# Kernel tuning notes

Hardware: AMD Instinct MI355X
Metric: run time of the kernel (lower is better)

Reference implementation:

```python
import jax, jax.numpy as jnp
import numpy as np

VOCAB = 50257
N_EMBD = 640
BLOCK = 256
B = 16


def setup_inputs() -> dict:
    key = jax.random.key(0)
    ks = jax.random.split(key, 8)
    std = 0.02
    return {
        "idx": jax.random.randint(ks[0], (B, BLOCK), 0, VOCAB, dtype=jnp.int64 if jax.config.jax_enable_x64 else jnp.int32),
        "w_embed": jax.random.normal(ks[1], (VOCAB, N_EMBD), jnp.float32) * std,
        "w_pos": jax.random.normal(ks[2], (BLOCK, N_EMBD), jnp.float32) * std,
        "wq": jax.random.normal(ks[3], (N_EMBD, N_EMBD), jnp.float32) * std,
        "wk": jax.random.normal(ks[4], (N_EMBD, N_EMBD), jnp.float32) * std,
        "wv": jax.random.normal(ks[5], (N_EMBD, N_EMBD), jnp.float32) * std,
        "w_out": jax.random.normal(ks[6], (VOCAB, N_EMBD), jnp.float32) * std,
        "b_out": jnp.zeros((VOCAB,), jnp.float32),
    }


def reference(idx, w_embed, w_pos, wq, wk, wv, w_out, b_out):
    # idx: (B, T) token ids. Dropout is identity (eval mode).
    Bt, T = idx.shape
    x = w_embed[idx] + w_pos[:T]                      # (B, T, D)
    q = jnp.einsum('btd,ed->bte', x, wq)              # torch Linear: x @ W.T
    k = jnp.einsum('btd,ed->bte', x, wk)
    v = jnp.einsum('btd,ed->bte', x, wv)
    scale = jnp.asarray(N_EMBD ** 0.5, x.dtype)
    scores = jnp.einsum('btd,bsd->bts', q, k) / scale  # (B, T, T)
    causal = jnp.triu(jnp.ones((T, T), bool), k=1)     # True above diagonal
    scores = jnp.where(causal, jnp.asarray(-jnp.inf, scores.dtype), scores)
    attn = jax.nn.softmax(scores, axis=-1)
    attn_out = jnp.einsum('bts,bsd->btd', attn, v)     # (B, T, D)
    logits = jnp.einsum('btd,vd->btv', attn_out, w_out) + b_out  # (B, T, V)
    return logits
```

## Files before the change

### kernel.cpp

```cpp
#include <hip/hip_runtime.h>
#include <hip/hip_bf16.h>
#include <stdint.h>

#define VOCAB 50257
#define VPAD  50432
#define DIM   640
#define SEQ   256
#define NBATCH 16
#define MROWS 4096

using bf16 = __hip_bfloat16;
typedef __attribute__((ext_vector_type(8))) short short8;
typedef __attribute__((ext_vector_type(4))) float f32x4;
struct bf16x4 { bf16 a, b, c, d; };

__device__ __forceinline__ void gld_lds16(const void* g, void* l) {
  __builtin_amdgcn_global_load_lds(
      (const __attribute__((address_space(1))) void*)g,
      (__attribute__((address_space(3))) void*)l, 16, 0, 0);
}

#define BAR() asm volatile("s_barrier" ::: "memory")
#define VMC0() asm volatile("s_waitcnt vmcnt(0)" ::: "memory")

__global__ void embed_kernel(const int* __restrict__ idx,
                             const float* __restrict__ we,
                             const float* __restrict__ wp,
                             bf16* __restrict__ xb) {
  int row = blockIdx.x;
  int t = row & (SEQ - 1);
  int tok = idx[row];
  const float* src = we + (long)tok * DIM;
  const float* pos = wp + (long)t * DIM;
  for (int d = threadIdx.x * 4; d < DIM; d += blockDim.x * 4) {
    float4 s = *(const float4*)(src + d);
    float4 p = *(const float4*)(pos + d);
    bf16x4 o = { __float2bfloat16(s.x + p.x), __float2bfloat16(s.y + p.y),
                 __float2bfloat16(s.z + p.z), __float2bfloat16(s.w + p.w) };
    *(bf16x4*)(xb + (long)row * DIM + d) = o;
  }
}

__global__ void conv4_kernel(const float* __restrict__ src, bf16* __restrict__ dst,
                             long n_src, long n_dst) {
  long i = ((long)blockIdx.x * blockDim.x + threadIdx.x) * 4;
  long stride = (long)gridDim.x * blockDim.x * 4;
  for (; i < n_dst; i += stride) {
    float4 v = (i < n_src) ? *(const float4*)(src + i) : make_float4(0.f, 0.f, 0.f, 0.f);
    bf16x4 o = { __float2bfloat16(v.x), __float2bfloat16(v.y),
                 __float2bfloat16(v.z), __float2bfloat16(v.w) };
    *(bf16x4*)(dst + i) = o;
  }
}

__global__ void transpose_v(const bf16* __restrict__ v, bf16* __restrict__ vt) {
  long i = (long)blockIdx.x * blockDim.x + threadIdx.x;
  if (i >= (long)NBATCH * DIM * SEQ) return;
  int t = (int)(i & (SEQ - 1));
  long be = i >> 8;
  int e = (int)(be % DIM);
  int b = (int)(be / DIM);
  vt[i] = v[((long)b * SEQ + t) * DIM + e];
}

__global__ void softmax_kernel(const float* __restrict__ sc, bf16* __restrict__ p) {
  int wid = threadIdx.x >> 6, lane = threadIdx.x & 63;
  int row = blockIdx.x * 4 + wid;
  int t = row & (SEQ - 1);
  const float* srow = sc + (long)row * SEQ;
  const float rsc = 0.03952847075210474f;
  float v[4];
  float mx = -1e30f;
#pragma unroll
  for (int i = 0; i < 4; ++i) {
    int s = lane + 64 * i;
    v[i] = (s <= t) ? srow[s] * rsc : -1e30f;
    mx = fmaxf(mx, v[i]);
  }
#pragma unroll
  for (int off = 32; off; off >>= 1) mx = fmaxf(mx, __shfl_xor(mx, off, 64));
  float sum = 0.f;
#pragma unroll
  for (int i = 0; i < 4; ++i) {
    int s = lane + 64 * i;
    v[i] = (s <= t) ? __expf(v[i] - mx) : 0.f;
    sum += v[i];
  }
#pragma unroll
  for (int off = 32; off; off >>= 1) sum += __shfl_xor(sum, off, 64);
  float inv = 1.f / sum;
#pragma unroll
  for (int i = 0; i < 4; ++i)
    p[(long)row * SEQ + lane + 64 * i] = __float2bfloat16(v[i] * inv);
}

template <int NT, typename OUT_T, bool BIAS>
__global__ __launch_bounds__(256, 4) void gemm_pipe(
    const bf16* __restrict__ Ag, const bf16* __restrict__ Bg,
    OUT_T* __restrict__ Cg, const float* __restrict__ bias,
    int K, int ldc, int Nstore, long sA, long sB, long sC) {
  __shared__ __align__(16) char lds[32768];
  const int tid = threadIdx.x;
  const int lane = tid & 63, wv = tid >> 6;
  const int lr = lane & 15, h16 = lane >> 4;

  const int tm = blockIdx.x, tn = blockIdx.y, bz = blockIdx.z;
  const bf16* A = Ag + (long)bz * sA + (long)tm * 128 * K;
  const bf16* B = Bg + (long)bz * sB + (long)tn * 128 * K;

  int srcE[2], dstW[2];
#pragma unroll
  for (int j = 0; j < 2; ++j) {
    int d = j * 256 + tid;
    int b = d ^ ((d >> 3) & 3);
    srcE[j] = (b >> 2) * K + (b & 3) * 8;
    dstW[j] = (j * 256 + wv * 64) * 16;
  }
  const bf16* aS0 = A + srcE[0];
  const bf16* aS1 = A + srcE[1];
  const bf16* bS0 = B + srcE[0];
  const bf16* bS1 = B + srcE[1];
  auto STAGE = [&](int slot, int t) {
    int kOff = t * 32;
    gld_lds16(aS0 + kOff, lds + slot + dstW[0]);
    gld_lds16(aS1 + kOff, lds + slot + dstW[1]);
    gld_lds16(bS0 + kOff, lds + slot + 8192 + dstW[0]);
    gld_lds16(bS1 + kOff, lds + slot + 8192 + dstW[1]);
  };

  const int wr = (wv >> 1) * 64, wc = (wv & 1) * 64;
  int aoff[4], boff[4];
#pragma unroll
  for (int m = 0; m < 4; ++m) {
    int La = (wr + m * 16 + lr) * 64 + h16 * 16;
    aoff[m] = La ^ (((La >> 7) & 3) << 4);
    int Lb = (wc + m * 16 + lr) * 64 + h16 * 16;
    boff[m] = 8192 + (Lb ^ (((Lb >> 7) & 3) << 4));
  }

  f32x4 acc[4][4] = {};
  short8 a[4], b[4];

  STAGE(0, 0);
  VMC0();
  BAR();

#pragma unroll 2
  for (int t = 0; t < NT; ++t) {
    const int cur = (t & 1) * 16384;
    if (t + 1 < NT) STAGE(16384 - cur, t + 1);
#pragma unroll
    for (int m = 0; m < 4; ++m) a[m] = *(const short8*)(lds + cur + aoff[m]);
#pragma unroll
    for (int n = 0; n < 4; ++n) b[n] = *(const short8*)(lds + cur + boff[n]);
    __builtin_amdgcn_s_setprio(1);
#pragma unroll
    for (int m = 0; m < 4; ++m)
#pragma unroll
      for (int n = 0; n < 4; ++n)
        acc[m][n] = __builtin_amdgcn_mfma_f32_16x16x32_bf16(a[m], b[n], acc[m][n], 0, 0, 0);
    __builtin_amdgcn_s_setprio(0);
    if (t + 1 < NT) VMC0();
    BAR();
  }

  if constexpr (sizeof(OUT_T) == 4) {
    float* Cf = (float*)Cg + (long)bz * sC;
    float bv[4];
#pragma unroll
    for (int n = 0; n < 4; ++n) {
      int col = tn * 128 + wc + lr + n * 16;
      bv[n] = (BIAS && col < Nstore) ? bias[col] : 0.f;
    }
    char* reg = lds + wv * 8192;
    const int rowL = lane & 31, cb = lane >> 5;
#pragma unroll
    for (int mm = 0; mm < 2; ++mm) {
#pragma unroll
      for (int mp = 0; mp < 2; ++mp)
#pragma unroll
        for (int n = 0; n < 4; ++n) {
          f32x4 v = acc[mm * 2 + mp][n];
          v[0] += bv[n]; v[1] += bv[n]; v[2] += bv[n]; v[3] += bv[n];
          int col = lr + n * 16;
          int rho = mp * 16 + h16 * 4;
          int w = col * 32 + (rho ^ ((col & 7) << 2));
          *(f32x4*)(reg + w * 4) = v;
        }
      const long rowg = tm * 128 + wr + mm * 32 + rowL;
#pragma unroll
      for (int k = 0; k < 8; ++k) {
        f32x4 o;
#pragma unroll
        for (int c = 0; c < 4; ++c) {
          int col = k * 8 + cb * 4 + c;
          int w = col * 32 + (rowL ^ ((col & 7) << 2));
          o[c] = *(const float*)(reg + w * 4);
        }
        int gcol = tn * 128 + wc + k * 8 + cb * 4;
        float* dst = Cf + rowg * (long)ldc + gcol;
        if (gcol + 3 < Nstore) {
          *(f32x4*)dst = o;
        } else {
#pragma unroll
          for (int c = 0; c < 4; ++c)
            if (gcol + c < Nstore) dst[c] = o[c];
        }
      }
    }
  } else {
    OUT_T* C = Cg + (long)bz * sC;
    const int crow0 = tm * 128 + wr + h16 * 4;
    const int ccol0 = tn * 128 + wc + lr;
#pragma unroll
    for (int m = 0; m < 4; ++m)
#pragma unroll
      for (int n = 0; n < 4; ++n) {
        int col = ccol0 + n * 16;
        if (col < Nstore) {
#pragma unroll
          for (int j = 0; j < 4; ++j) {
            long row = crow0 + m * 16 + j;
            C[row * ldc + col] = __float2bfloat16(acc[m][n][j]);
          }
        }
      }
  }
}

__global__ __launch_bounds__(1024, 4) void gemm_v(
    const bf16* __restrict__ Ag, const bf16* __restrict__ Bg,
    float* __restrict__ Cg, const float* __restrict__ bias) {
  __shared__ __align__(16) char lds[65536];
  const int tid = threadIdx.x;
  const int lane = tid & 63, wv = tid >> 6;
  const int lr = lane & 15, h16 = lane >> 4;
  const int wm = wv >> 2, wn = wv & 3;

  const int tm = blockIdx.x, tn = blockIdx.y;
  const bf16* A = Ag + (long)tm * 256 * DIM;
  const bf16* B = Bg + (long)tn * 256 * DIM;

  int srcE, dstW;
  {
    int d = tid;
    int b = d ^ ((d >> 3) & 3);
    srcE = (b >> 2) * DIM + (b & 3) * 8;
    dstW = wv * 1024;
  }
  const bf16* aS = A + srcE;
  const bf16* bS = B + srcE;
  auto STAGE = [&](int slot, int t) {
    int kOff = t * 32;
    gld_lds16(aS + kOff, lds + slot + dstW);
    gld_lds16(bS + kOff, lds + slot + 16384 + dstW);
  };

  int aoff[4], boff[4];
#pragma unroll
  for (int m = 0; m < 4; ++m) {
    int La = (wm * 64 + m * 16 + lr) * 64 + h16 * 16;
    aoff[m] = La ^ (((La >> 7) & 3) << 4);
    int Lb = (wn * 64 + m * 16 + lr) * 64 + h16 * 16;
    boff[m] = 16384 + (Lb ^ (((Lb >> 7) & 3) << 4));
  }

  f32x4 acc[4][4] = {};
  short8 a[4], b[4];

  STAGE(0, 0);
  VMC0();
  BAR();

#pragma unroll 2
  for (int t = 0; t < 20; ++t) {
    const int cur = (t & 1) * 32768;
    if (t + 1 < 20) STAGE(32768 - cur, t + 1);
#pragma unroll
    for (int m = 0; m < 4; ++m) a[m] = *(const short8*)(lds + cur + aoff[m]);
#pragma unroll
    for (int n = 0; n < 4; ++n) b[n] = *(const short8*)(lds + cur + boff[n]);
    __builtin_amdgcn_s_setprio(1);
#pragma unroll
    for (int m = 0; m < 4; ++m)
#pragma unroll
      for (int n = 0; n < 4; ++n)
        acc[m][n] = __builtin_amdgcn_mfma_f32_16x16x32_bf16(a[m], b[n], acc[m][n], 0, 0, 0);
    __builtin_amdgcn_s_setprio(0);
    if (t + 1 < 20) VMC0();
    BAR();
  }

  const int crow0 = tm * 256 + wm * 64 + h16 * 4;
  const int ccol0 = tn * 256 + wn * 64 + lr;
  float bv[4];
#pragma unroll
  for (int n = 0; n < 4; ++n) {
    int col = ccol0 + n * 16;
    bv[n] = (col < VOCAB) ? bias[col] : 0.f;
  }
#pragma unroll
  for (int m = 0; m < 4; ++m)
#pragma unroll
    for (int n = 0; n < 4; ++n) {
      int col = ccol0 + n * 16;
      if (col < VOCAB) {
#pragma unroll
        for (int j = 0; j < 4; ++j)
          Cg[(long)(crow0 + m * 16 + j) * VOCAB + col] = acc[m][n][j] + bv[n];
      }
    }
}

extern "C" void kernel_launch(void* const* d_in, const int* in_sizes, int n_in,
                              void* d_out, int out_size, void* d_ws, size_t ws_size,
                              hipStream_t stream) {
  const int*   idx     = (const int*)d_in[0];
  const float* w_embed = (const float*)d_in[1];
  const float* w_pos   = (const float*)d_in[2];
  const float* wq      = (const float*)d_in[3];
  const float* wk      = (const float*)d_in[4];
  const float* wv      = (const float*)d_in[5];
  const float* w_out   = (const float*)d_in[6];
  const float* b_out   = (const float*)d_in[7];
  float* out = (float*)d_out;

  size_t off = 0;
  auto alloc = [&](size_t bytes) {
    void* p = (char*)d_ws + off;
    off += (bytes + 255) & ~(size_t)255;
    return p;
  };
  bf16* x_bf    = (bf16*)alloc((size_t)MROWS * DIM * 2);
  bf16* wqkv_bf = (bf16*)alloc((size_t)3 * DIM * DIM * 2);
  bf16* wout_bf = (bf16*)alloc((size_t)VPAD * DIM * 2);
  bf16* qkv     = (bf16*)alloc((size_t)3 * MROWS * DIM * 2);
  bf16* vT      = (bf16*)alloc((size_t)NBATCH * DIM * SEQ * 2);
  float* scores = (float*)alloc((size_t)NBATCH * SEQ * SEQ * 4);
  bf16* P       = (bf16*)alloc((size_t)NBATCH * SEQ * SEQ * 2);
  bf16* attn    = (bf16*)alloc((size_t)MROWS * DIM * 2);

  const long QKV_S = (long)MROWS * DIM;
  const long W_S   = (long)DIM * DIM;

  embed_kernel<<<MROWS, 256, 0, stream>>>(idx, w_embed, w_pos, x_bf);

  conv4_kernel<<<256, 256, 0, stream>>>(wq, wqkv_bf,           W_S, W_S);
  conv4_kernel<<<256, 256, 0, stream>>>(wk, wqkv_bf + W_S,     W_S, W_S);
  conv4_kernel<<<256, 256, 0, stream>>>(wv, wqkv_bf + 2 * W_S, W_S, W_S);
  conv4_kernel<<<2048, 256, 0, stream>>>(w_out, wout_bf, (long)VOCAB * DIM, (long)VPAD * DIM);

  gemm_pipe<20, bf16, false><<<dim3(MROWS / 128, DIM / 128, 3), 256, 0, stream>>>(
      x_bf, wqkv_bf, qkv, nullptr, DIM, DIM, DIM, 0, W_S, QKV_S);

  {
    long n = (long)NBATCH * DIM * SEQ;
    transpose_v<<<(int)((n + 255) / 256), 256, 0, stream>>>(qkv + 2 * QKV_S, vT);
  }

  gemm_pipe<20, float, false><<<dim3(SEQ / 128, SEQ / 128, NBATCH), 256, 0, stream>>>(
      qkv, qkv + QKV_S, scores, nullptr, DIM, SEQ, SEQ,
      (long)SEQ * DIM, (long)SEQ * DIM, (long)SEQ * SEQ);

  softmax_kernel<<<MROWS / 4, 256, 0, stream>>>(scores, P);

  gemm_pipe<8, bf16, false><<<dim3(SEQ / 128, DIM / 128, NBATCH), 256, 0, stream>>>(
      P, vT, attn, nullptr, SEQ, DIM, DIM,
      (long)SEQ * SEQ, (long)DIM * SEQ, (long)SEQ * DIM);

  gemm_v<<<dim3(MROWS / 256, VPAD / 256), 1024, 0, stream>>>(attn, wout_bf, out, b_out);
}
```

Measured before the change: 668.9 us.

## Retile output-projection GEMM to 64x512 tiles with 512-thread blocks

Replaces the 256x256-tile, 1024-thread vocab-projection GEMM with a 64-row by 512-column tile using 8 waves. Each wave now covers the full 64 rows and its own 64-column slice, and the vocab padding grows to a multiple of 512. The intent is to change the tile shape and grid so that the A tile is small and shared across waves, with more blocks for better occupancy and wave balance. The cost is less reuse of A per loaded B column and more B traffic per block.

```diff
diff --git a/kernel.cpp b/kernel.cpp
--- a/kernel.cpp
+++ b/kernel.cpp
@@ -3,7 +3,7 @@
 #include <stdint.h>
 
 #define VOCAB 50257
-#define VPAD  50432
+#define VPAD2 50688
 #define DIM   640
 #define SEQ   256
 #define NBATCH 16
@@ -228,41 +228,48 @@
   }
 }
 
-__global__ __launch_bounds__(1024, 4) void gemm_v(
+__global__ __launch_bounds__(512, 4) void gemm_w(
     const bf16* __restrict__ Ag, const bf16* __restrict__ Bg,
     float* __restrict__ Cg, const float* __restrict__ bias) {
-  __shared__ __align__(16) char lds[65536];
+  __shared__ __align__(16) char lds[73728];
   const int tid = threadIdx.x;
   const int lane = tid & 63, wv = tid >> 6;
   const int lr = lane & 15, h16 = lane >> 4;
-  const int wm = wv >> 2, wn = wv & 3;
 
   const int tm = blockIdx.x, tn = blockIdx.y;
-  const bf16* A = Ag + (long)tm * 256 * DIM;
-  const bf16* B = Bg + (long)tn * 256 * DIM;
-
-  int srcE, dstW;
+  const bf16* A = Ag + (long)tm * 64 * DIM;
+  const bf16* B = Bg + (long)tn * 512 * DIM;
+
+  int srcA, dstA;
   {
-    int d = tid;
+    int d = tid & 255;
     int b = d ^ ((d >> 3) & 3);
-    srcE = (b >> 2) * DIM + (b & 3) * 8;
-    dstW = wv * 1024;
-  }
-  const bf16* aS = A + srcE;
-  const bf16* bS = B + srcE;
+    srcA = (b >> 2) * DIM + (b & 3) * 8;
+    dstA = ((wv & 3) * 64) * 16;
+  }
+  int srcB[4], dstB[4];
+#pragma unroll
+  for (int j = 0; j < 4; ++j) {
+    int d = j * 512 + tid;
+    int b = d ^ ((d >> 3) & 3);
+    srcB[j] = (b >> 2) * DIM + (b & 3) * 8;
+    dstB[j] = (j * 512 + wv * 64) * 16;
+  }
   auto STAGE = [&](int slot, int t) {
     int kOff = t * 32;
-    gld_lds16(aS + kOff, lds + slot + dstW);
-    gld_lds16(bS + kOff, lds + slot + 16384 + dstW);
+    if (tid < 256) gld_lds16(A + srcA + kOff, lds + slot + dstA);
+#pragma unroll
+    for (int j = 0; j < 4; ++j)
+      gld_lds16(B + srcB[j] + kOff, lds + slot + 4096 + dstB[j]);
   };
 
   int aoff[4], boff[4];
 #pragma unroll
   for (int m = 0; m < 4; ++m) {
-    int La = (wm * 64 + m * 16 + lr) * 64 + h16 * 16;
+    int La = (m * 16 + lr) * 64 + h16 * 16;
     aoff[m] = La ^ (((La >> 7) & 3) << 4);
-    int Lb = (wn * 64 + m * 16 + lr) * 64 + h16 * 16;
-    boff[m] = 16384 + (Lb ^ (((Lb >> 7) & 3) << 4));
+    int Lb = (wv * 64 + m * 16 + lr) * 64 + h16 * 16;
+    boff[m] = 4096 + (Lb ^ (((Lb >> 7) & 3) << 4));
   }
 
   f32x4 acc[4][4] = {};
@@ -274,8 +281,8 @@
 
 #pragma unroll 2
   for (int t = 0; t < 20; ++t) {
-    const int cur = (t & 1) * 32768;
-    if (t + 1 < 20) STAGE(32768 - cur, t + 1);
+    const int cur = (t & 1) * 36864;
+    if (t + 1 < 20) STAGE(36864 - cur, t + 1);
 #pragma unroll
     for (int m = 0; m < 4; ++m) a[m] = *(const short8*)(lds + cur + aoff[m]);
 #pragma unroll
@@ -291,8 +298,8 @@
     BAR();
   }
 
-  const int crow0 = tm * 256 + wm * 64 + h16 * 4;
-  const int ccol0 = tn * 256 + wn * 64 + lr;
+  const int crow0 = tm * 64 + h16 * 4;
+  const int ccol0 = tn * 512 + wv * 64 + lr;
   float bv[4];
 #pragma unroll
   for (int n = 0; n < 4; ++n) {
@@ -333,7 +340,7 @@
   };
   bf16* x_bf    = (bf16*)alloc((size_t)MROWS * DIM * 2);
   bf16* wqkv_bf = (bf16*)alloc((size_t)3 * DIM * DIM * 2);
-  bf16* wout_bf = (bf16*)alloc((size_t)VPAD * DIM * 2);
+  bf16* wout_bf = (bf16*)alloc((size_t)VPAD2 * DIM * 2);
   bf16* qkv     = (bf16*)alloc((size_t)3 * MROWS * DIM * 2);
   bf16* vT      = (bf16*)alloc((size_t)NBATCH * DIM * SEQ * 2);
   float* scores = (float*)alloc((size_t)NBATCH * SEQ * SEQ * 4);
@@ -348,7 +355,7 @@
   conv4_kernel<<<256, 256, 0, stream>>>(wq, wqkv_bf,           W_S, W_S);
   conv4_kernel<<<256, 256, 0, stream>>>(wk, wqkv_bf + W_S,     W_S, W_S);
   conv4_kernel<<<256, 256, 0, stream>>>(wv, wqkv_bf + 2 * W_S, W_S, W_S);
-  conv4_kernel<<<2048, 256, 0, stream>>>(w_out, wout_bf, (long)VOCAB * DIM, (long)VPAD * DIM);
+  conv4_kernel<<<2048, 256, 0, stream>>>(w_out, wout_bf, (long)VOCAB * DIM, (long)VPAD2 * DIM);
 
   gemm_pipe<20, bf16, false><<<dim3(MROWS / 128, DIM / 128, 3), 256, 0, stream>>>(
       x_bf, wqkv_bf, qkv, nullptr, DIM, DIM, DIM, 0, W_S, QKV_S);
@@ -368,5 +375,5 @@
       P, vT, attn, nullptr, SEQ, DIM, DIM,
       (long)SEQ * SEQ, (long)DIM * SEQ, (long)SEQ * DIM);
 
-  gemm_v<<<dim3(MROWS / 256, VPAD / 256), 1024, 0, stream>>>(attn, wout_bf, out, b_out);
-}
+  gemm_w<<<dim3(MROWS / 64, VPAD2 / 512), 512, 0, stream>>>(attn, wout_bf, out, b_out);
+}
```

New measurement: 770.7 us. 1.15x slower.
